# Kernel tuning notes

Measured on AMD Instinct MI355X. Metric: run time of the kernel, lower is better.

The kernel has to match this reference:

```python
import jax, jax.numpy as jnp
import numpy as np

B, H, T, D = 2, 16, 2048, 64
R1, R2 = 4, 8


def setup_inputs() -> dict:
    key = jax.random.key(0)
    ks = jax.random.split(key, 7)
    return {
        "q": jax.random.normal(ks[0], (B, H, T, D), dtype=jnp.float32),
        "k": jax.random.normal(ks[1], (B, H, T, D), dtype=jnp.float32),
        "v": jax.random.normal(ks[2], (B, H, T, D), dtype=jnp.float32),
        "W_q": jax.random.normal(ks[3], (H, D, R1 * R2), dtype=jnp.float32) / np.sqrt(D),
        "W_k": jax.random.normal(ks[4], (H, D, R1 * R2), dtype=jnp.float32) / np.sqrt(D),
        "core1": jax.random.normal(ks[5], (H, R1), dtype=jnp.float32),
        "core2": jax.random.normal(ks[6], (H, R2), dtype=jnp.float32),
    }


def reference(q, k, v, W_q, W_k, core1, core2):
    """Kronecker low-rank (LSR) causal attention.

    scores[b,h,m,n] = (1/sqrt(R1*R2)) * sum_r kron[h,r] * (q@W_q)[b,h,m,r] * (k@W_k)[b,h,n,r]
    where kron[h] = core1[h] (x) core2[h]  (per-head Kronecker product).
    """
    Hh, r1 = core1.shape
    r2 = core2.shape[1]
    # per-head Kronecker core vector: (H, R1*R2)
    kron = (core1[:, :, None] * core2[:, None, :]).reshape(Hh, r1 * r2)
    scale = 1.0 / jnp.sqrt(jnp.float32(r1 * r2))
    # low-rank projections, rank R = R1*R2
    q_lr = jnp.einsum("bhtd,hdr->bhtr", q, W_q) * kron[None, :, None, :]  # [B,H,T,R]
    k_lr = jnp.einsum("bhtd,hdr->bhtr", k, W_k)                            # [B,H,T,R]
    scores = jnp.einsum("bhmr,bhnr->bhmn", q_lr, k_lr) * scale             # [B,H,T,T]
    t = q.shape[2]
    causal = jnp.tril(jnp.ones((t, t), dtype=bool))
    scores = jnp.where(causal[None, None], scores, -jnp.inf)
    p = jax.nn.softmax(scores, axis=-1)
    return jnp.einsum("bhmn,bhnd->bhmd", p, v)
```

## Files before the change

kernel.cpp:

```cpp
#include <hip/hip_runtime.h>

typedef _Float16 f16;
typedef _Float16 f16x2 __attribute__((ext_vector_type(2)));
typedef _Float16 f16x4 __attribute__((ext_vector_type(4)));
typedef _Float16 f16x8 __attribute__((ext_vector_type(8)));
typedef float    f32x4 __attribute__((ext_vector_type(4)));
typedef float    f32x16 __attribute__((ext_vector_type(16)));

constexpr int B_ = 2, H_ = 16, T_ = 2048, D_ = 64, R_ = 32, NT = 32;
constexpr int NROW = B_ * H_ * T_;

__device__ __forceinline__ f32x4 mfma16(f16x8 a, f16x8 b, f32x4 c) {
  return __builtin_amdgcn_mfma_f32_16x16x32_f16(a, b, c, 0, 0, 0);
}
__device__ __forceinline__ f32x16 mfma32(f16x8 a, f16x8 b, f32x16 c) {
  return __builtin_amdgcn_mfma_f32_32x32x16_f16(a, b, c, 0, 0, 0);
}
__device__ __forceinline__ void ld_lds16(const void* g, void* l) {
  __builtin_amdgcn_global_load_lds(
      (const __attribute__((address_space(1))) unsigned int*)g,
      (__attribute__((address_space(3))) unsigned int*)l, 16, 0, 0);
}

__global__ __launch_bounds__(256) void proj_kernel(
    const float* __restrict__ q, const float* __restrict__ k, const float* __restrict__ v,
    const float* __restrict__ Wq, const float* __restrict__ Wk,
    const float* __restrict__ c1, const float* __restrict__ c2,
    f16* __restrict__ qlr, f16* __restrict__ klr, f16* __restrict__ vt)
{
  __shared__ float sv[64 * 65];

  const int tid = threadIdx.x, w = tid >> 6, lane = tid & 63;
  const int l15 = lane & 15, l4 = lane >> 4;
  const int bh = blockIdx.x >> 5, h = bh & (H_ - 1);
  const int t0 = (blockIdx.x & 31) * 64;

  const float* vb = v + ((size_t)bh * T_ + t0) * D_;
  float4 vld[4];
#pragma unroll
  for (int it = 0; it < 4; ++it) vld[it] = ((const float4*)vb)[it * 256 + tid];

  const int m = t0 + 16 * w + l15;
  const float* qr = q + ((size_t)bh * T_ + m) * D_;
  const float* kr = k + ((size_t)bh * T_ + m) * D_;
  f16x8 aq[2], ak[2];
#pragma unroll
  for (int kc = 0; kc < 2; ++kc) {
    float4 x0 = *(const float4*)(qr + kc * 32 + 8 * l4);
    float4 x1 = *(const float4*)(qr + kc * 32 + 8 * l4 + 4);
    float4 y0 = *(const float4*)(kr + kc * 32 + 8 * l4);
    float4 y1 = *(const float4*)(kr + kc * 32 + 8 * l4 + 4);
    f16x8 A, K;
    A[0]=(f16)x0.x; A[1]=(f16)x0.y; A[2]=(f16)x0.z; A[3]=(f16)x0.w;
    A[4]=(f16)x1.x; A[5]=(f16)x1.y; A[6]=(f16)x1.z; A[7]=(f16)x1.w;
    K[0]=(f16)y0.x; K[1]=(f16)y0.y; K[2]=(f16)y0.z; K[3]=(f16)y0.w;
    K[4]=(f16)y1.x; K[5]=(f16)y1.y; K[6]=(f16)y1.z; K[7]=(f16)y1.w;
    aq[kc] = A; ak[kc] = K;
  }

  const float* Wqh = Wq + (size_t)h * D_ * R_;
  const float* Wkh = Wk + (size_t)h * D_ * R_;
  f16x8 bq[2][2], bk[2][2];
#pragma unroll
  for (int kc = 0; kc < 2; ++kc)
#pragma unroll
    for (int nt = 0; nt < 2; ++nt) {
      const int r = 16 * nt + l15;
      f16x8 q8, k8;
#pragma unroll
      for (int j2 = 0; j2 < 8; ++j2) {
        const int d = kc * 32 + 8 * l4 + j2;
        q8[j2] = (f16)Wqh[d * R_ + r];
        k8[j2] = (f16)Wkh[d * R_ + r];
      }
      bq[kc][nt] = q8; bk[kc][nt] = k8;
    }

#pragma unroll
  for (int it = 0; it < 4; ++it) {
    const int i4 = it * 256 + tid, t = i4 >> 4, dq = (i4 & 15) * 4;
    sv[t * 65 + dq    ] = vld[it].x;
    sv[t * 65 + dq + 1] = vld[it].y;
    sv[t * 65 + dq + 2] = vld[it].z;
    sv[t * 65 + dq + 3] = vld[it].w;
  }

  const f32x4 z4 = {0.f, 0.f, 0.f, 0.f};
#pragma unroll
  for (int nt = 0; nt < 2; ++nt) {
    f32x4 accq = mfma16(aq[0], bq[0][nt], z4);
    accq = mfma16(aq[1], bq[1][nt], accq);
    f32x4 acck = mfma16(ak[0], bk[0][nt], z4);
    acck = mfma16(ak[1], bk[1][nt], acck);
    const int r = 16 * nt + l15;
    const float scl = c1[h * 4 + (r >> 3)] * c2[h * 8 + (r & 7)] *
                      (0.17677669529663687f * 1.4426950408889634f);
#pragma unroll
    for (int i = 0; i < 4; ++i) {
      const size_t row = (size_t)bh * T_ + t0 + 16 * w + 4 * l4 + i;
      qlr[row * R_ + r] = (f16)(accq[i] * scl);
      klr[row * R_ + r] = (f16)acck[i];
    }
  }

  __syncthreads();
#pragma unroll
  for (int it = 0; it < 8; ++it) {
    const int idx = it * 256 + tid, d = idx >> 5, t = (idx & 31) * 2;
    const float f0 = sv[t * 65 + d], f1 = sv[t * 65 + 65 + d];
    f16x2 pr; pr[0] = (f16)f0; pr[1] = (f16)f1;
    const int sw = ((((t >> 3) ^ (d & 7)) << 3) | (t & 7));
    *(f16x2*)(vt + ((size_t)bh * D_ + d) * T_ + t0 + sw) = pr;
  }
}


__device__ __forceinline__ void compute_tile(
    const f16* __restrict__ sk, const f16* __restrict__ svt, f16* __restrict__ sp,
    const f16x8 aq0, const f16x8 aq1, const bool diag,
    float& mi0, float& mi1, float& li0, float& li1, f32x16* oacc,
    const int w, const int lane)
{
  const int l15 = lane & 15, l4 = lane >> 4, l31 = lane & 31, hh = lane >> 5;
  const f32x4 z4 = {0.f, 0.f, 0.f, 0.f};

  f32x4 sc[4][2];
#pragma unroll
  for (int ns = 0; ns < 4; ++ns) {
    f16x8 akf = *(const f16x8*)&sk[(16 * ns + l15) * 32 + 8 * l4];
    sc[ns][0] = mfma16(akf, aq0, z4);
    sc[ns][1] = mfma16(akf, aq1, z4);
  }
  if (diag) {
    const int lim0 = 32 * w + l15;
#pragma unroll
    for (int ns = 0; ns < 4; ++ns) {
      const int nb = 16 * ns + 4 * l4;
#pragma unroll
      for (int i = 0; i < 4; ++i) {
        if (nb + i > lim0)      sc[ns][0][i] = -1e30f;
        if (nb + i > lim0 + 16) sc[ns][1][i] = -1e30f;
      }
    }
  }

  float rm0 = -1e30f, rm1 = -1e30f;
#pragma unroll
  for (int ns = 0; ns < 4; ++ns)
#pragma unroll
    for (int i = 0; i < 4; ++i) {
      rm0 = fmaxf(rm0, sc[ns][0][i]);
      rm1 = fmaxf(rm1, sc[ns][1][i]);
    }
  rm0 = fmaxf(rm0, __shfl_xor(rm0, 16)); rm0 = fmaxf(rm0, __shfl_xor(rm0, 32));
  rm1 = fmaxf(rm1, __shfl_xor(rm1, 16)); rm1 = fmaxf(rm1, __shfl_xor(rm1, 32));
  const float mn0 = fmaxf(mi0, rm0), mn1 = fmaxf(mi1, rm1);
  const float a0 = exp2f(mi0 - mn0), a1 = exp2f(mi1 - mn1);
  float rs0 = 0.f, rs1 = 0.f;
#pragma unroll
  for (int ns = 0; ns < 4; ++ns) {
    f16x4 p0v, p1v;
#pragma unroll
    for (int i = 0; i < 4; ++i) {
      const float p0 = exp2f(sc[ns][0][i] - mn0);
      const float p1 = exp2f(sc[ns][1][i] - mn1);
      rs0 += p0; rs1 += p1;
      p0v[i] = (f16)p0; p1v[i] = (f16)p1;
    }
    const int col = ((((2 * ns + (l4 >> 1)) ^ (l15 & 7)) << 3) | (4 * (l4 & 1)));
    *(f16x4*)&sp[l15 * 64 + col]        = p0v;
    *(f16x4*)&sp[(16 + l15) * 64 + col] = p1v;
  }
  rs0 += __shfl_xor(rs0, 16); rs0 += __shfl_xor(rs0, 32);
  rs1 += __shfl_xor(rs1, 16); rs1 += __shfl_xor(rs1, 32);
  li0 = li0 * a0 + rs0; li1 = li1 * a1 + rs1;
  mi0 = mn0; mi1 = mn1;
  const float aPV = (lane & 16) ? a1 : a0;
#pragma unroll
  for (int c = 0; c < 2; ++c) oacc[c] *= aPV;

#pragma unroll
  for (int kc = 0; kc < 4; ++kc) {
    const int u = (2 * kc + hh) ^ (l31 & 7);
    f16x8 bp = *(const f16x8*)&sp[l31 * 64 + u * 8];
#pragma unroll
    for (int c = 0; c < 2; ++c) {
      f16x8 av = *(const f16x8*)&svt[(32 * c + l31) * 64 + u * 8];
      oacc[c] = mfma32(av, bp, oacc[c]);
    }
  }
}

__device__ __forceinline__ void write_out(
    f16* __restrict__ On, float2* __restrict__ ml, const size_t base,
    const f32x16* oacc, const float mi0, const float mi1,
    const float li0, const float li1, const int w, const int lane)
{
  const int l15 = lane & 15, l4 = lane >> 4, l31 = lane & 31, hh = lane >> 5;
  const float myl = (lane & 16) ? li1 : li0;
  const float invl = myl > 0.f ? 1.f / myl : 0.f;
  f16* ob = On + (base + 32 * w + l31) * D_;
#pragma unroll
  for (int c = 0; c < 2; ++c)
#pragma unroll
    for (int g = 0; g < 4; ++g) {
      f16x4 o;
#pragma unroll
      for (int e = 0; e < 4; ++e) o[e] = (f16)(oacc[c][4 * g + e] * invl);
      *(f16x4*)(ob + 32 * c + 8 * g + 4 * hh) = o;
    }
  if (l4 < 2) {
    float2 mlv;
    mlv.x = l4 ? mi1 : mi0;
    mlv.y = l4 ? li1 : li0;
    ml[base + 32 * w + 16 * l4 + l15] = mlv;
  }
}

__global__ __launch_bounds__(128) void attn_kernel(
    const f16* __restrict__ qlr, const f16* __restrict__ klr,
    const f16* __restrict__ vt, f16* __restrict__ On, float2* __restrict__ ml,
    const int NS)
{
  __shared__ __align__(16) f16 s_k[2][64 * 32];
  __shared__ __align__(16) f16 s_vt[2][64 * 64];
  __shared__ __align__(16) f16 s_p[2][32 * 64];

  const int tid = threadIdx.x, w = tid >> 6, lane = tid & 63;
  const int l15 = lane & 15, l4 = lane >> 4;
  const int bh = blockIdx.x & 31;
  const int rest = blockIdx.x >> 5;
  const int s  = rest & (NS - 1);
  const int pr = (NS == 2) ? (rest >> 1) : rest;
  const int mtA = pr, mtB = 31 - pr;
  const int m0A = mtA * 64, m0B = mtB * 64;

  const f16x8 aqA0 = *(const f16x8*)(qlr + ((size_t)bh * T_ + m0A + 32 * w + l15) * R_ + 8 * l4);
  const f16x8 aqA1 = *(const f16x8*)(qlr + ((size_t)bh * T_ + m0A + 32 * w + 16 + l15) * R_ + 8 * l4);
  const f16x8 aqB0 = *(const f16x8*)(qlr + ((size_t)bh * T_ + m0B + 32 * w + l15) * R_ + 8 * l4);
  const f16x8 aqB1 = *(const f16x8*)(qlr + ((size_t)bh * T_ + m0B + 32 * w + 16 + l15) * R_ + 8 * l4);

  const f16* kb = klr + (size_t)bh * T_ * R_;
  const f16* vb = vt + (size_t)bh * D_ * T_;

  f32x16 oA[2], oB[2];
#pragma unroll
  for (int c = 0; c < 2; ++c)
#pragma unroll
    for (int e = 0; e < 16; ++e) { oA[c][e] = 0.f; oB[c][e] = 0.f; }
  float miA0 = -1e30f, miA1 = -1e30f, liA0 = 0.f, liA1 = 0.f;
  float miB0 = -1e30f, miB1 = -1e30f, liB0 = 0.f, liB1 = 0.f;

  auto stage = [&](int bf, int j) {
    const int n0 = 64 * j;
#pragma unroll
    for (int e = 0; e < 2; ++e)
      ld_lds16((const char*)kb + (size_t)n0 * 64 + (2 * w + e) * 1024 + lane * 16,
               (char*)(&s_k[bf][0]) + (2 * w + e) * 1024);
#pragma unroll
    for (int e = 0; e < 4; ++e) {
      const int d0 = w * 32 + e * 8;
      ld_lds16((const char*)vb + ((size_t)(d0 + (lane >> 3)) * T_ + n0) * 2 + (lane & 7) * 16,
               (char*)(&s_vt[bf][0]) + d0 * 128);
    }
  };

  stage(0, s);
  __syncthreads();
  int buf = 0;
  for (int j = s; j <= mtB; j += NS) {
    const int jn = j + NS;
    if (jn <= mtB) stage(buf ^ 1, jn);
    if (j <= mtA)
      compute_tile(&s_k[buf][0], &s_vt[buf][0], &s_p[w][0], aqA0, aqA1, j == mtA,
                   miA0, miA1, liA0, liA1, oA, w, lane);
    compute_tile(&s_k[buf][0], &s_vt[buf][0], &s_p[w][0], aqB0, aqB1, j == mtB,
                 miB0, miB1, liB0, liB1, oB, w, lane);
    __syncthreads();
    buf ^= 1;
  }

  const size_t baseA = ((size_t)s * 32 + bh) * T_ + m0A;
  const size_t baseB = ((size_t)s * 32 + bh) * T_ + m0B;
  write_out(On, ml, baseA, oA, miA0, miA1, liA0, liA1, w, lane);
  write_out(On, ml, baseB, oB, miB0, miB1, liB0, liB1, w, lane);
}

__global__ __launch_bounds__(256) void merge_kernel(
    const f16* __restrict__ On, const float2* __restrict__ ml,
    float* __restrict__ out, const int NS)
{
  const int row = blockIdx.x * 32 + (threadIdx.x >> 3);
  const int d0 = (threadIdx.x & 7) * 8;
  const f16x8 o0 = *(const f16x8*)(On + (size_t)row * 64 + d0);
  float res[8];
  if (NS == 2) {
    const float2 a = ml[row];
    const float2 b = ml[NROW + row];
    const f16x8 o1 = *(const f16x8*)(On + ((size_t)NROW + row) * 64 + d0);
    const float ms = fmaxf(a.x, b.x);
    const float w0 = exp2f(a.x - ms) * a.y;
    const float w1 = exp2f(b.x - ms) * b.y;
    const float inv = 1.f / (w0 + w1);
    const float c0 = w0 * inv, c1 = w1 * inv;
#pragma unroll
    for (int e = 0; e < 8; ++e) res[e] = c0 * (float)o0[e] + c1 * (float)o1[e];
  } else {
#pragma unroll
    for (int e = 0; e < 8; ++e) res[e] = (float)o0[e];
  }
  float* ob = out + (size_t)row * 64 + d0;
  f32x4 r0, r1;
#pragma unroll
  for (int e = 0; e < 4; ++e) { r0[e] = res[e]; r1[e] = res[4 + e]; }
  *(f32x4*)ob = r0;
  *(f32x4*)(ob + 4) = r1;
}

extern "C" void kernel_launch(void* const* d_in, const int* in_sizes, int n_in,
                              void* d_out, int out_size, void* d_ws, size_t ws_size,
                              hipStream_t stream) {
  const float* q  = (const float*)d_in[0];
  const float* k  = (const float*)d_in[1];
  const float* v  = (const float*)d_in[2];
  const float* Wq = (const float*)d_in[3];
  const float* Wk = (const float*)d_in[4];
  const float* c1 = (const float*)d_in[5];
  const float* c2 = (const float*)d_in[6];
  float* out = (float*)d_out;

  f16* qlr = (f16*)d_ws;
  f16* klr = qlr + (size_t)B_ * H_ * T_ * R_;
  f16* vt  = klr + (size_t)B_ * H_ * T_ * R_;
  f16* On  = vt + (size_t)B_ * H_ * T_ * D_;
  float2* ml = (float2*)(On + (size_t)2 * NROW * D_);

  const int NS = (ws_size >= ((size_t)33 * 1024 * 1024 + (1 << 20))) ? 2 : 1;

  proj_kernel<<<B_ * H_ * NT, 256, 0, stream>>>(q, k, v, Wq, Wk, c1, c2, qlr, klr, vt);
  attn_kernel<<<32 * 16 * NS, 128, 0, stream>>>(qlr, klr, vt, On, ml, NS);
  merge_kernel<<<NROW / 32, 256, 0, stream>>>(On, ml, out, NS);
}
```

Baseline: 154.4 us.

## Split attention KV range four ways and single-buffer LDS for occupancy

Raises the number of key-sequence splits from two to four when the workspace allows, so four times as many attention blocks run, each over a quarter of the key tiles. The merge kernel gains a four-way log-sum-exp combine. LDS double buffering is replaced by a single buffer with a sync before and after each load, and launch bounds request four blocks per CU, trading load/compute overlap for higher occupancy. It also adds more partial-output traffic and merge work.

```diff
diff --git a/kernel.cpp b/kernel.cpp
--- a/kernel.cpp
+++ b/kernel.cpp
@@ -217,21 +217,21 @@
   }
 }
 
-__global__ __launch_bounds__(128) void attn_kernel(
+__global__ __launch_bounds__(128, 4) void attn_kernel(
     const f16* __restrict__ qlr, const f16* __restrict__ klr,
     const f16* __restrict__ vt, f16* __restrict__ On, float2* __restrict__ ml,
     const int NS)
 {
-  __shared__ __align__(16) f16 s_k[2][64 * 32];
-  __shared__ __align__(16) f16 s_vt[2][64 * 64];
+  __shared__ __align__(16) f16 s_k[64 * 32];
+  __shared__ __align__(16) f16 s_vt[64 * 64];
   __shared__ __align__(16) f16 s_p[2][32 * 64];
 
   const int tid = threadIdx.x, w = tid >> 6, lane = tid & 63;
   const int l15 = lane & 15, l4 = lane >> 4;
   const int bh = blockIdx.x & 31;
   const int rest = blockIdx.x >> 5;
-  const int s  = rest & (NS - 1);
-  const int pr = (NS == 2) ? (rest >> 1) : rest;
+  const int pr = rest / NS;
+  const int s  = rest - pr * NS;
   const int mtA = pr, mtB = 31 - pr;
   const int m0A = mtA * 64, m0B = mtB * 64;
 
@@ -251,33 +251,26 @@
   float miA0 = -1e30f, miA1 = -1e30f, liA0 = 0.f, liA1 = 0.f;
   float miB0 = -1e30f, miB1 = -1e30f, liB0 = 0.f, liB1 = 0.f;
 
-  auto stage = [&](int bf, int j) {
+  for (int j = s; j <= mtB; j += NS) {
     const int n0 = 64 * j;
+    __syncthreads();
 #pragma unroll
     for (int e = 0; e < 2; ++e)
       ld_lds16((const char*)kb + (size_t)n0 * 64 + (2 * w + e) * 1024 + lane * 16,
-               (char*)(&s_k[bf][0]) + (2 * w + e) * 1024);
+               (char*)s_k + (2 * w + e) * 1024);
 #pragma unroll
     for (int e = 0; e < 4; ++e) {
       const int d0 = w * 32 + e * 8;
       ld_lds16((const char*)vb + ((size_t)(d0 + (lane >> 3)) * T_ + n0) * 2 + (lane & 7) * 16,
-               (char*)(&s_vt[bf][0]) + d0 * 128);
-    }
-  };
-
-  stage(0, s);
-  __syncthreads();
-  int buf = 0;
-  for (int j = s; j <= mtB; j += NS) {
-    const int jn = j + NS;
-    if (jn <= mtB) stage(buf ^ 1, jn);
+               (char*)s_vt + d0 * 128);
+    }
+    __syncthreads();
+
     if (j <= mtA)
-      compute_tile(&s_k[buf][0], &s_vt[buf][0], &s_p[w][0], aqA0, aqA1, j == mtA,
+      compute_tile(s_k, s_vt, &s_p[w][0], aqA0, aqA1, j == mtA,
                    miA0, miA1, liA0, liA1, oA, w, lane);
-    compute_tile(&s_k[buf][0], &s_vt[buf][0], &s_p[w][0], aqB0, aqB1, j == mtB,
+    compute_tile(s_k, s_vt, &s_p[w][0], aqB0, aqB1, j == mtB,
                  miB0, miB1, liB0, liB1, oB, w, lane);
-    __syncthreads();
-    buf ^= 1;
   }
 
   const size_t baseA = ((size_t)s * 32 + bh) * T_ + m0A;
@@ -292,11 +285,30 @@
 {
   const int row = blockIdx.x * 32 + (threadIdx.x >> 3);
   const int d0 = (threadIdx.x & 7) * 8;
-  const f16x8 o0 = *(const f16x8*)(On + (size_t)row * 64 + d0);
   float res[8];
-  if (NS == 2) {
+  if (NS == 4) {
+    const float2 a0 = ml[row];
+    const float2 a1 = ml[1 * NROW + row];
+    const float2 a2 = ml[2 * NROW + row];
+    const float2 a3 = ml[3 * NROW + row];
+    const f16x8 o0 = *(const f16x8*)(On + (size_t)row * 64 + d0);
+    const f16x8 o1 = *(const f16x8*)(On + ((size_t)1 * NROW + row) * 64 + d0);
+    const f16x8 o2 = *(const f16x8*)(On + ((size_t)2 * NROW + row) * 64 + d0);
+    const f16x8 o3 = *(const f16x8*)(On + ((size_t)3 * NROW + row) * 64 + d0);
+    const float ms = fmaxf(fmaxf(a0.x, a1.x), fmaxf(a2.x, a3.x));
+    const float w0 = exp2f(a0.x - ms) * a0.y;
+    const float w1 = exp2f(a1.x - ms) * a1.y;
+    const float w2 = exp2f(a2.x - ms) * a2.y;
+    const float w3 = exp2f(a3.x - ms) * a3.y;
+    const float inv = 1.f / (w0 + w1 + w2 + w3);
+    const float c0 = w0 * inv, c1 = w1 * inv, c2 = w2 * inv, c3 = w3 * inv;
+#pragma unroll
+    for (int e = 0; e < 8; ++e)
+      res[e] = c0 * (float)o0[e] + c1 * (float)o1[e] + c2 * (float)o2[e] + c3 * (float)o3[e];
+  } else if (NS == 2) {
     const float2 a = ml[row];
     const float2 b = ml[NROW + row];
+    const f16x8 o0 = *(const f16x8*)(On + (size_t)row * 64 + d0);
     const f16x8 o1 = *(const f16x8*)(On + ((size_t)NROW + row) * 64 + d0);
     const float ms = fmaxf(a.x, b.x);
     const float w0 = exp2f(a.x - ms) * a.y;
@@ -306,6 +318,7 @@
 #pragma unroll
     for (int e = 0; e < 8; ++e) res[e] = c0 * (float)o0[e] + c1 * (float)o1[e];
   } else {
+    const f16x8 o0 = *(const f16x8*)(On + (size_t)row * 64 + d0);
 #pragma unroll
     for (int e = 0; e < 8; ++e) res[e] = (float)o0[e];
   }
@@ -329,13 +342,16 @@
   const float* c2 = (const float*)d_in[6];
   float* out = (float*)d_out;
 
+  const size_t MB = 1 << 20;
+  int NS = 1;
+  if (ws_size >= 16 * MB + 4 * (8 * MB + NROW * sizeof(float2))) NS = 4;
+  else if (ws_size >= 16 * MB + 2 * (8 * MB + NROW * sizeof(float2))) NS = 2;
+
   f16* qlr = (f16*)d_ws;
   f16* klr = qlr + (size_t)B_ * H_ * T_ * R_;
   f16* vt  = klr + (size_t)B_ * H_ * T_ * R_;
   f16* On  = vt + (size_t)B_ * H_ * T_ * D_;
-  float2* ml = (float2*)(On + (size_t)2 * NROW * D_);
-
-  const int NS = (ws_size >= ((size_t)33 * 1024 * 1024 + (1 << 20))) ? 2 : 1;
+  float2* ml = (float2*)(On + (size_t)NS * NROW * D_);
 
   proj_kernel<<<B_ * H_ * NT, 256, 0, stream>>>(q, k, v, Wq, Wk, c1, c2, qlr, klr, vt);
   attn_kernel<<<32 * 16 * NS, 128, 0, stream>>>(qlr, klr, vt, On, ml, NS);
```

Measured after the change: 189.0 us. 1.22x slower.
